# Kernel optimization log

Hardware: AMD Instinct MI355X
Metric: run time of the kernel (lower is better)

## Reference

```python
import jax, jax.numpy as jnp
import numpy as np

STEP = 2  # neighbor window size (init arg `step`)


def _shift_sums(x, step):
    # sum over shifted-left (before) and shifted-right (after) neighbor states,
    # zero-padded at the boundaries, for shifts 1..step. x: [B, L, H]
    before = sum(jnp.pad(x[:, :-s, :], ((0, 0), (s, 0), (0, 0))) for s in range(1, step + 1))
    after = sum(jnp.pad(x[:, s:, :], ((0, 0), (0, s), (0, 0))) for s in range(1, step + 1))
    return before, after


def _slstm_forward(word_inputs, mask, num_layers, init_h, init_c, Wx, Wh, Wi, Wd, b, gWx, gWh, gb):
    B, L, D = word_inputs.shape
    H = Wx.shape[-1]
    fm = mask.astype(word_inputs.dtype)          # [B, L]
    seq_mask = fm[:, :, None]                    # [B, L, 1]
    mask_score = (fm * 1e25 - 1e25)[:, :, None]  # -inf-like for padded positions

    emb = word_inputs * seq_mask                 # embedding_hidden_state_pre
    h = (init_h * 0.1 - 0.05) * seq_mask         # uniform(-0.05, 0.05) init
    c = (init_c * 0.1 - 0.05) * seq_mask
    dh = jnp.mean(h, axis=1)                     # dummy-node hidden [B, H]
    dc = jnp.mean(c, axis=1)                     # dummy-node cell   [B, H]

    for _ in range(num_layers):
        comb = jnp.mean(h, axis=1)               # combined word hidden [B, H]
        dh_rep = jnp.broadcast_to(dh[:, None, :], (B, L, H))
        dc_rep = jnp.broadcast_to(dc[:, None, :], (B, L, H))

        # --- dummy (sentence) node update ---
        g_d = jax.nn.sigmoid(dh @ gWx[0] + comb @ gWh[0] + gb[0])              # [B, H]
        g_o = jax.nn.sigmoid(dh @ gWx[1] + comb @ gWh[1] + gb[1])              # [B, H]
        g_f = jax.nn.sigmoid(dh_rep @ gWx[2] + h @ gWh[2] + gb[2])             # [B, L, H]
        scores = jnp.concatenate([g_f + mask_score, g_d[:, None, :]], axis=1)  # [B, L+1, H]
        scores = jax.nn.softmax(scores, axis=1)
        dummy_c = jnp.sum(scores[:, :L, :] * c, axis=1) + scores[:, L, :] * dc
        dummy_h = g_o * jnp.tanh(dummy_c)

        # --- word node updates ---
        hb, ha = _shift_sums(h, STEP)
        cb, ca = _shift_sums(c, STEP)
        cat_h = jnp.concatenate([hb, ha], axis=-1)  # [B, L, 2H]

        # 7 gates stacked: f1, f2, f3, f4, i, o, u -> pre: [7, B, L, H]
        pre = (jnp.einsum('blh,ghk->gblk', h, Wx)
               + jnp.einsum('blh,ghk->gblk', cat_h, Wh)
               + jnp.einsum('bld,gdk->gblk', emb, Wi)
               + jnp.einsum('blh,ghk->gblk', dh_rep, Wd)
               + b[:, None, None, :])
        sig = jax.nn.sigmoid(pre[:6])
        f1, f2, f3, f4, i_g, o_g = sig[0], sig[1], sig[2], sig[3], sig[4], sig[5]
        u = jnp.tanh(pre[6])

        # normalize the five forget/input gates via softmax across gates
        five = jax.nn.softmax(jnp.stack([f1, f2, f3, f4, i_g], axis=0), axis=0)
        c_new = five[0] * cb + five[1] * ca + five[2] * c + five[3] * dc_rep + five[4] * u
        h_new = o_g * jnp.tanh(c_new)

        h = h_new * seq_mask
        c = c_new * seq_mask
        dh, dc = dummy_h, dummy_c

    return h


def setup_inputs() -> dict:
    key = jax.random.key(0)
    ks = jax.random.split(key, 12)
    B, L, D, H, G = 32, 1024, 256, 256, 7
    s = 0.1  # stddev of param init in the torch module
    return {
        'word_inputs': jax.random.normal(ks[0], (B, L, D), jnp.float32),
        'mask': jnp.ones((B, L), jnp.int32),
        'num_layers': 3,
        'init_h': jax.random.uniform(ks[1], (B, L, H), jnp.float32),
        'init_c': jax.random.uniform(ks[2], (B, L, H), jnp.float32),
        'Wx': jax.random.normal(ks[3], (G, H, H), jnp.float32) * s,
        'Wh': jax.random.normal(ks[4], (G, 2 * H, H), jnp.float32) * s,
        'Wi': jax.random.normal(ks[5], (G, D, H), jnp.float32) * s,
        'Wd': jax.random.normal(ks[6], (G, H, H), jnp.float32) * s,
        'b': jax.random.normal(ks[7], (G, H), jnp.float32) * s,
        'gWx': jax.random.normal(ks[8], (3, H, H), jnp.float32) * s,
        'gWh': jax.random.normal(ks[9], (3, H, H), jnp.float32) * s,
        'gb': jax.random.normal(ks[10], (3, H), jnp.float32) * s,
    }


def reference(word_inputs, mask, num_layers, init_h, init_c, Wx, Wh, Wi, Wd, b, gWx, gWh, gb):
    return _slstm_forward(word_inputs, mask, num_layers, init_h, init_c, Wx, Wh, Wi, Wd, b, gWx, gWh, gb)
```

## Files before the change

kernel.cpp:

```cpp
#include <hip/hip_runtime.h>
#include <hip/hip_bf16.h>
#include <math.h>

#define BB 32
#define LL 1024
#define DD 256
#define HH 256
#define NG 7
#define HW (HH*HH)
#define WhS (2*HH*HH)

typedef short bf16x8 __attribute__((ext_vector_type(8)));
typedef float f32x4  __attribute__((ext_vector_type(4)));
typedef unsigned short u16;
typedef unsigned int u32;

__device__ __forceinline__ float sigm(float x){ return 1.0f/(1.0f + expf(-x)); }
__device__ __forceinline__ float fsig(float x){ return __fdividef(1.0f, 1.0f + __expf(-x)); }
__device__ __forceinline__ float ftanh(float x){ return 1.0f - __fdividef(2.0f, 1.0f + __expf(2.0f*x)); }
__device__ __forceinline__ u16 f2b(float f){
  u32 u = __float_as_uint(f);
  return (u16)((u + 0x7fffu + ((u>>16)&1u)) >> 16);
}
__device__ __forceinline__ float b2f(u16 b){ return __uint_as_float(((u32)b)<<16); }
__device__ __forceinline__ float4 ld4(const float* p){ return *reinterpret_cast<const float4*>(p); }
__device__ __forceinline__ u32 packf2(float lo, float hi){
  float2 s; s.x = lo; s.y = hi;
  __hip_bfloat162 r = __float22bfloat162_rn(s);
  return *reinterpret_cast<u32*>(&r);
}
__device__ __forceinline__ u32 bfadd2(u32 a, u32 b){
  float lo = __uint_as_float(a << 16)        + __uint_as_float(b << 16);
  float hi = __uint_as_float(a & 0xffff0000u) + __uint_as_float(b & 0xffff0000u);
  return packf2(lo, hi);
}

__device__ __forceinline__ void gload16(const void* g, void* l){
  __builtin_amdgcn_global_load_lds(
    (const __attribute__((address_space(1))) unsigned int*)g,
    (__attribute__((address_space(3))) unsigned int*)l, 16, 0, 0);
}
__device__ __forceinline__ f32x4 mfma16(bf16x8 a, bf16x8 b, f32x4 c){
  return __builtin_amdgcn_mfma_f32_16x16x32_bf16(a, b, c, 0, 0, 0);
}

__global__ __launch_bounds__(256) void k_init(const float* __restrict__ ih, const float* __restrict__ ic,
    const int* __restrict__ mask, u16* __restrict__ h, float* __restrict__ c){
  size_t n = (size_t)BB*LL*HH;
  for (size_t idx = (size_t)blockIdx.x*256 + threadIdx.x; idx < n; idx += (size_t)gridDim.x*256){
    float fm = (float)mask[idx>>8];
    h[idx] = f2b((ih[idx]*0.1f - 0.05f)*fm);
    c[idx] = (ic[idx]*0.1f - 0.05f)*fm;
  }
}

__global__ __launch_bounds__(256) void k_embpack(const float* __restrict__ win,
    const int* __restrict__ mask, u16* __restrict__ embp){
  int idx = blockIdx.x*256 + threadIdx.x;
  int m = idx >> 5, c8 = (idx & 31) << 3;
  float fm = (float)mask[m];
  float4 w0 = ld4(win + (size_t)m*DD + c8);
  float4 w1 = ld4(win + (size_t)m*DD + c8 + 4);
  uint4 pv;
  pv.x = packf2(w0.x*fm, w0.y*fm); pv.y = packf2(w0.z*fm, w0.w*fm);
  pv.z = packf2(w1.x*fm, w1.y*fm); pv.w = packf2(w1.z*fm, w1.w*fm);
  *(uint4*)(embp + (size_t)m*HH + c8) = pv;
}

__global__ __launch_bounds__(256) void k_mean1(const u16* __restrict__ h, const float* __restrict__ c,
    float* __restrict__ pmh, float* __restrict__ pmc){
  int b = blockIdx.x, ch = blockIdx.y, k = threadIdx.x;
  const u16* hp = h + ((size_t)b*LL + ch*64)*HH + k;
  const float* cp = c + ((size_t)b*LL + ch*64)*HH + k;
  float sh = 0.f, sc = 0.f;
  for (int l = 0; l < 64; ++l){ sh += b2f(hp[(size_t)l*HH]); sc += cp[(size_t)l*HH]; }
  pmh[(size_t)(b*16+ch)*HH + k] = sh;
  pmc[(size_t)(b*16+ch)*HH + k] = sc;
}
__global__ __launch_bounds__(256) void k_mean2(const float* __restrict__ pmh, const float* __restrict__ pmc,
    float* __restrict__ comb, float* __restrict__ combc){
  int b = blockIdx.x, k = threadIdx.x;
  float sh = 0.f, sc = 0.f;
  for (int ch = 0; ch < 16; ++ch){
    sh += pmh[(size_t)(b*16+ch)*HH + k];
    sc += pmc[(size_t)(b*16+ch)*HH + k];
  }
  comb[b*HH+k]  = sh*(1.0f/LL);
  combc[b*HH+k] = sc*(1.0f/LL);
}

__global__ __launch_bounds__(256) void k_small(const float* __restrict__ dh, const float* __restrict__ comb,
    const float* __restrict__ gWx, const float* __restrict__ gWh, const float* __restrict__ gb,
    const float* __restrict__ Wd, const float* __restrict__ bias,
    float* __restrict__ g_d, float* __restrict__ g_o, float* __restrict__ gx2f, float* __restrict__ wd){
  __shared__ float dsh[HH], csh[HH];
  int b = blockIdx.x, g = blockIdx.y, k = threadIdx.x;
  dsh[k] = dh[b*HH+k]; csh[k] = comb[b*HH+k];
  __syncthreads();
  if (g < NG){
    float aw = bias[g*HH+k];
    const float* W = Wd + (size_t)g*HW + k;
    for (int j = 0; j < HH; ++j) aw += dsh[j]*W[(size_t)j*HH];
    wd[(size_t)(g*BB + b)*HH + k] = aw;
  } else {
    float ad = gb[0*HH+k], ao = gb[1*HH+k], ax = gb[2*HH+k];
    for (int j = 0; j < HH; ++j){
      float dv = dsh[j], cv = csh[j];
      ad += dv*gWx[j*HH+k]      + cv*gWh[j*HH+k];
      ao += dv*gWx[HW + j*HH+k] + cv*gWh[HW + j*HH+k];
      ax += dv*gWx[2*HW + j*HH+k];
    }
    g_d[b*HH+k] = sigm(ad);
    g_o[b*HH+k] = sigm(ao);
    gx2f[b*HH+k] = ax;
  }
}

__global__ __launch_bounds__(256) void k_wpack(const float* __restrict__ Wx, const float* __restrict__ Wh,
    const float* __restrict__ Wi, u16* __restrict__ Bp){
  int idx = blockIdx.x*256 + threadIdx.x;
  int img = idx / 14336, e = idx % 14336;
  int nt = img >> 5, ks = img & 31;
  int g = e >> 11, r = e & 2047;
  int n = r >> 5, kblk = (r>>3)&3, j = r&7;
  int K = ks*32 + kblk*8 + j;
  int N = nt*64 + n;
  int slice = K >> 8, kr = K & 255;
  float v;
  if (slice == 0)      v = Wx[(size_t)g*HW  + (size_t)kr*HH + N];
  else if (slice == 1) v = Wh[(size_t)g*WhS + (size_t)kr*HH + N];
  else if (slice == 2) v = Wh[(size_t)g*WhS + (size_t)(256+kr)*HH + N];
  else                 v = Wi[(size_t)g*HW  + (size_t)kr*HH + N];
  Bp[idx] = f2b(v);
}

__global__ __launch_bounds__(256) void k_gw2pack(const float* __restrict__ gWh, u16* __restrict__ Gp){
  int idx = blockIdx.x*256 + threadIdx.x;
  int img = idx >> 11, r = idx & 2047;
  int nt = img >> 3, ks = img & 7;
  int n = r >> 5, kblk = (r>>3)&3, j = r&7;
  int K = ks*32 + kblk*8 + j, N = nt*64 + n;
  Gp[idx] = f2b(gWh[2*HW + (size_t)K*HH + N]);
}

__global__ __launch_bounds__(256) void k_dummy2(const float* __restrict__ pnumP, const float* __restrict__ pdenP,
    const float* __restrict__ g_d, const float* __restrict__ g_o, const float* __restrict__ dc,
    float* __restrict__ dh_n, float* __restrict__ dc_n){
  int b = blockIdx.x, k = threadIdx.x;
  float num = 0.f, den = 0.f;
  for (int mt = 0; mt < 16; ++mt){
    num += pnumP[(size_t)(b*16+mt)*HH + k];
    den += pdenP[(size_t)(b*16+mt)*HH + k];
  }
  float ed = expf(g_d[b*HH+k]);
  float v = (num + ed*dc[b*HH+k])/(den + ed);
  dc_n[b*HH+k] = v;
  dh_n[b*HH+k] = g_o[b*HH+k]*tanhf(v);
}

__global__ __launch_bounds__(256, 2) void k_main(const u16* __restrict__ h,
    const float* __restrict__ c, const u16* __restrict__ embp,
    const int* __restrict__ mask,
    const u16* __restrict__ Bp, const u16* __restrict__ Gp,
    const float* __restrict__ wd, const float* __restrict__ dc,
    const float* __restrict__ gx2f,
    u16* __restrict__ hout, float* __restrict__ cout, float* __restrict__ hf32,
    float* __restrict__ pnumP, float* __restrict__ pdenP, int wf32, int wc){
  __shared__ __align__(16) unsigned char lsA[3][4][4096];

  int tid = threadIdx.x, lane = tid & 63, wid = tid >> 6;
  int flat = blockIdx.x;
  int xcd = flat & 7, q = flat >> 3;
  int nt  = xcd >> 1;
  int mt  = (xcd & 1)*256 + q;
  int m0 = mt << 6, b = m0 >> 10;
  int li = lane & 15, kg = lane >> 4;

  int rA = wid*16 + (lane>>2); (void)rA;
  int kbA = (lane&3) ^ ((lane>>3)&3);
  int mA = m0 + wid*16 + (lane>>2), lpA = mA & (LL-1);

  int off0 = li*64 + ((kg ^ ((li>>1)&3))<<4);

  const unsigned char* bbase = (const unsigned char*)Bp
      + (size_t)nt*32*28672 + (size_t)(wid*16+li)*64 + (size_t)kg*16;
  const unsigned char* gbase = (const unsigned char*)Gp
      + (size_t)nt*8*4096  + (size_t)(wid*16+li)*64 + (size_t)kg*16;

  f32x4 acc[NG][4];
  f32x4 acc8[4];
  #pragma unroll
  for (int g=0; g<NG; ++g)
    #pragma unroll
    for (int mf=0; mf<4; ++mf) acc[g][mf] = (f32x4)0.f;
  #pragma unroll
  for (int mf=0; mf<4; ++mf) acc8[mf] = (f32x4)0.f;

  auto stage = [&](int Gs, int dst){
    int base = 4*Gs, s1 = base >> 3;
    if (s1 == 0 || s1 == 3){
      const u16* src = (s1 == 0) ? h : embp;
      #pragma unroll
      for (int j=0;j<4;++j)
        gload16(src + (size_t)mA*HH + ((base+j)&7)*32 + kbA*8, lsA[dst][j] + wid*1024);
    } else {
      int d = (s1 == 1) ? -(int)HH : (int)HH;
      bool e1 = (s1 == 1) ? (lpA >= 1) : (lpA <= LL-2);
      bool e2 = (s1 == 1) ? (lpA >= 2) : (lpA <= LL-3);
      #pragma unroll
      for (int j=0;j<4;++j){
        int co = ((base+j)&7)*32 + kbA*8;
        const u16* hp = h + (size_t)mA*HH + co;
        uint4 u1 = e1 ? *(const uint4*)(hp + d)   : make_uint4(0,0,0,0);
        uint4 u2 = e2 ? *(const uint4*)(hp + 2*d) : make_uint4(0,0,0,0);
        uint4 pv;
        pv.x = bfadd2(u1.x,u2.x); pv.y = bfadd2(u1.y,u2.y);
        pv.z = bfadd2(u1.z,u2.z); pv.w = bfadd2(u1.w,u2.w);
        *(uint4*)(lsA[dst][j] + wid*1024 + lane*16) = pv;
      }
    }
  };

  stage(0, 0);
  stage(1, 1);
  asm volatile("s_waitcnt vmcnt(4)" ::: "memory");
  __builtin_amdgcn_s_barrier();

  #pragma unroll 1
  for (int G = 0; G < 8; ++G){
    if (G < 6) stage(G+2, (G+2)%3);
    int setc = G % 3;
    #pragma unroll
    for (int j = 0; j < 4; ++j){
      int ks = 4*G + j;
      const unsigned char* bstep = bbase + (size_t)ks*28672;
      bf16x8 bg[NG];
      #pragma unroll
      for (int g = 0; g < NG; ++g) bg[g] = *(const bf16x8*)(bstep + g*4096);
      bf16x8 aa[4];
      #pragma unroll
      for (int mf=0; mf<4; ++mf)
        aa[mf] = *(const bf16x8*)(lsA[setc][j] + mf*1024 + off0);
      __builtin_amdgcn_s_setprio(1);
      #pragma unroll
      for (int g = 0; g < NG; ++g)
        #pragma unroll
        for (int mf=0; mf<4; ++mf) acc[g][mf] = mfma16(aa[mf], bg[g], acc[g][mf]);
      if (ks < 8){
        bf16x8 b8 = *(const bf16x8*)(gbase + (size_t)ks*4096);
        #pragma unroll
        for (int mf=0; mf<4; ++mf) acc8[mf] = mfma16(aa[mf], b8, acc8[mf]);
      }
      __builtin_amdgcn_s_setprio(0);
    }
    asm volatile("s_waitcnt vmcnt(4)" ::: "memory");
    __builtin_amdgcn_s_barrier();
  }

  int col = nt*64 + wid*16 + li;
  float wdv[NG];
  #pragma unroll
  for (int g=0; g<NG; ++g) wdv[g] = wd[(size_t)(g*BB+b)*HH + col];
  float dcv = dc[b*HH + col];
  float gx  = gx2f[b*HH + col];
  float num = 0.f, den = 0.f;

  #pragma unroll
  for (int mf=0; mf<4; ++mf)
  #pragma unroll
  for (int j=0; j<4; ++j){
    int m = m0 + mf*16 + kg*4 + j;
    int lp = m & (LL-1);
    float fm = (float)mask[m];
    const float* cp = c + (size_t)m*HH + col;
    float cc = cp[0];
    float cbv = 0.f, cav = 0.f;
    if (lp >= 1)    cbv += cp[-(int)HH];
    if (lp >= 2)    cbv += cp[-2*(int)HH];
    if (lp <= LL-2) cav += cp[HH];
    if (lp <= LL-3) cav += cp[2*HH];
    float s0 = fsig(acc[0][mf][j] + wdv[0]);
    float s1 = fsig(acc[1][mf][j] + wdv[1]);
    float s2 = fsig(acc[2][mf][j] + wdv[2]);
    float s3 = fsig(acc[3][mf][j] + wdv[3]);
    float s4 = fsig(acc[4][mf][j] + wdv[4]);
    float s5 = fsig(acc[5][mf][j] + wdv[5]);
    float u  = ftanh(acc[6][mf][j] + wdv[6]);
    float e0 = __expf(s0), e1 = __expf(s1), e2 = __expf(s2), e3 = __expf(s3), e4 = __expf(s4);
    float inv = __fdividef(1.0f, e0+e1+e2+e3+e4);
    float cn = (e0*cbv + e1*cav + e2*cc + e3*dcv + e4*u)*inv;
    float hn = s5*ftanh(cn);
    hout[(size_t)m*HH + col] = f2b(hn*fm);
    if (wc)   cout[(size_t)m*HH + col] = cn*fm;
    if (wf32) hf32[(size_t)m*HH + col] = hn*fm;
    float s8 = fsig(acc8[mf][j] + gx);
    float e8 = fm * __expf(s8);
    num += e8 * cc;
    den += e8;
  }
  num += __shfl_xor(num, 16); num += __shfl_xor(num, 32);
  den += __shfl_xor(den, 16); den += __shfl_xor(den, 32);
  if (kg == 0){
    pnumP[(size_t)(m0>>6)*HH + col] = num;
    pdenP[(size_t)(m0>>6)*HH + col] = den;
  }
}

extern "C" void kernel_launch(void* const* d_in, const int* in_sizes, int n_in,
                              void* d_out, int out_size, void* d_ws, size_t ws_size,
                              hipStream_t stream) {
  const float* win   = (const float*)d_in[0];
  const int*   mask  = (const int*)d_in[1];
  const float* ih    = (const float*)d_in[3];
  const float* ic    = (const float*)d_in[4];
  const float* Wx    = (const float*)d_in[5];
  const float* Wh    = (const float*)d_in[6];
  const float* Wi    = (const float*)d_in[7];
  const float* Wd    = (const float*)d_in[8];
  const float* bias  = (const float*)d_in[9];
  const float* gWx   = (const float*)d_in[10];
  const float* gWh   = (const float*)d_in[11];
  const float* gb    = (const float*)d_in[12];

  const size_t SZ = (size_t)BB*LL*HH;
  char* p = (char*)d_ws;
  auto alloc = [&](size_t bytes)->char*{ char* r = p; p += (bytes + 255) & ~(size_t)255; return r; };
  u16*   hA    = (u16*)  alloc(SZ*2);
  u16*   hB    = (u16*)  alloc(SZ*2);
  float* cA    = (float*)alloc(SZ*4);
  float* cB    = (float*)d_out;
  u16*   embp  = (u16*)  alloc(SZ*2);
  u16*   Bp    = (u16*)  alloc((size_t)1835008*2);
  u16*   Gp    = (u16*)  alloc((size_t)65536*2);
  float* comb  = (float*)alloc(BB*HH*4);
  float* combc = (float*)alloc(BB*HH*4);
  float* dh0   = (float*)alloc(BB*HH*4);
  float* dh1   = (float*)alloc(BB*HH*4);
  float* dc0   = (float*)alloc(BB*HH*4);
  float* dc1   = (float*)alloc(BB*HH*4);
  float* g_d   = (float*)alloc(BB*HH*4);
  float* g_o   = (float*)alloc(BB*HH*4);
  float* gx2f  = (float*)alloc(BB*HH*4);
  float* wd    = (float*)alloc((size_t)NG*BB*HH*4);
  float* pnumP = (float*)alloc((size_t)512*HH*4);
  float* pdenP = (float*)alloc((size_t)512*HH*4);
  float* pmh   = (float*)alloc((size_t)BB*16*HH*4);
  float* pmc   = (float*)alloc((size_t)BB*16*HH*4);
  float* dhb[2] = {dh0, dh1};
  float* dcb[2] = {dc0, dc1};

  k_wpack<<<7168, 256, 0, stream>>>(Wx, Wh, Wi, Bp);
  k_gw2pack<<<256, 256, 0, stream>>>(gWh, Gp);
  k_embpack<<<4096, 256, 0, stream>>>(win, mask, embp);
  k_init<<<2048, 256, 0, stream>>>(ih, ic, mask, hA, cA);

  u16 *h_cur = hA, *h_nxt = hB;
  float *c_cur = cA, *c_nxt = cB;
  for (int layer = 0; layer < 3; ++layer){
    k_mean1<<<dim3(BB,16), 256, 0, stream>>>(h_cur, c_cur, pmh, pmc);
    k_mean2<<<BB, 256, 0, stream>>>(pmh, pmc, comb, combc);
    const float* dh_l = (layer == 0) ? comb  : dhb[(layer+1)&1];
    const float* dc_l = (layer == 0) ? combc : dcb[(layer+1)&1];
    k_small<<<dim3(BB,8), 256, 0, stream>>>(dh_l, comb, gWx, gWh, gb, Wd, bias, g_d, g_o, gx2f, wd);
    int last = (layer == 2);
    k_main<<<2048, 256, 0, stream>>>(h_cur, c_cur, embp, mask, Bp, Gp, wd, dc_l, gx2f,
                                     h_nxt, c_nxt, (float*)d_out, pnumP, pdenP, last, !last);
    k_dummy2<<<BB, 256, 0, stream>>>(pnumP, pdenP, g_d, g_o, dc_l, dhb[layer&1], dcb[layer&1]);
    u16* th = h_cur; h_cur = h_nxt; h_nxt = th;
    float* tc = c_cur; c_cur = c_nxt; c_nxt = tc;
  }
}
```

Baseline: 694.9 us.

## Fuse sequence-mean reductions into init and main kernels, drop mean kernels

Column partial sums of h and c over sequence positions are now produced inside k_init and in the k_main epilogue through wave shuffles, so the separate k_mean1/k_mean2 passes that reread the full h and c tensors each layer are gone. The final reduction of the partials moves into the small gate kernel, now k_ms. This saves a full read of h (bf16) and c (fp32) per layer plus two launches. In exchange k_main gets two extra shuffle reductions and stores, and the layer-1+ mean is summed from fp32 values rather than from rounded bf16 h, which changes numerics slightly.

```diff
diff --git a/kernel.cpp b/kernel.cpp
--- a/kernel.cpp
+++ b/kernel.cpp
@@ -45,13 +45,22 @@
 }
 
 __global__ __launch_bounds__(256) void k_init(const float* __restrict__ ih, const float* __restrict__ ic,
-    const int* __restrict__ mask, u16* __restrict__ h, float* __restrict__ c){
-  size_t n = (size_t)BB*LL*HH;
-  for (size_t idx = (size_t)blockIdx.x*256 + threadIdx.x; idx < n; idx += (size_t)gridDim.x*256){
-    float fm = (float)mask[idx>>8];
-    h[idx] = f2b((ih[idx]*0.1f - 0.05f)*fm);
-    c[idx] = (ic[idx]*0.1f - 0.05f)*fm;
-  }
+    const int* __restrict__ mask, u16* __restrict__ h, float* __restrict__ c,
+    float* __restrict__ pmh, float* __restrict__ pmc){
+  int b = blockIdx.x, ch = blockIdx.y, k = threadIdx.x;
+  size_t base = ((size_t)b*LL + ch*64)*HH + k;
+  float sh = 0.f, sc = 0.f;
+  for (int l = 0; l < 64; ++l){
+    size_t idx = base + (size_t)l*HH;
+    float fm = (float)mask[b*LL + ch*64 + l];
+    float hv = (ih[idx]*0.1f - 0.05f)*fm;
+    float cv = (ic[idx]*0.1f - 0.05f)*fm;
+    h[idx] = f2b(hv);
+    c[idx] = cv;
+    sh += hv; sc += cv;
+  }
+  pmh[(size_t)(b*16+ch)*HH + k] = sh;
+  pmc[(size_t)(b*16+ch)*HH + k] = sc;
 }
 
 __global__ __launch_bounds__(256) void k_embpack(const float* __restrict__ win,
@@ -67,35 +76,19 @@
   *(uint4*)(embp + (size_t)m*HH + c8) = pv;
 }
 
-__global__ __launch_bounds__(256) void k_mean1(const u16* __restrict__ h, const float* __restrict__ c,
-    float* __restrict__ pmh, float* __restrict__ pmc){
-  int b = blockIdx.x, ch = blockIdx.y, k = threadIdx.x;
-  const u16* hp = h + ((size_t)b*LL + ch*64)*HH + k;
-  const float* cp = c + ((size_t)b*LL + ch*64)*HH + k;
-  float sh = 0.f, sc = 0.f;
-  for (int l = 0; l < 64; ++l){ sh += b2f(hp[(size_t)l*HH]); sc += cp[(size_t)l*HH]; }
-  pmh[(size_t)(b*16+ch)*HH + k] = sh;
-  pmc[(size_t)(b*16+ch)*HH + k] = sc;
-}
-__global__ __launch_bounds__(256) void k_mean2(const float* __restrict__ pmh, const float* __restrict__ pmc,
-    float* __restrict__ comb, float* __restrict__ combc){
-  int b = blockIdx.x, k = threadIdx.x;
-  float sh = 0.f, sc = 0.f;
-  for (int ch = 0; ch < 16; ++ch){
-    sh += pmh[(size_t)(b*16+ch)*HH + k];
-    sc += pmc[(size_t)(b*16+ch)*HH + k];
-  }
-  comb[b*HH+k]  = sh*(1.0f/LL);
-  combc[b*HH+k] = sc*(1.0f/LL);
-}
-
-__global__ __launch_bounds__(256) void k_small(const float* __restrict__ dh, const float* __restrict__ comb,
+__global__ __launch_bounds__(256) void k_ms(const float* __restrict__ pmh, const float* __restrict__ pmc,
+    const float* __restrict__ dh_in,
     const float* __restrict__ gWx, const float* __restrict__ gWh, const float* __restrict__ gb,
     const float* __restrict__ Wd, const float* __restrict__ bias,
-    float* __restrict__ g_d, float* __restrict__ g_o, float* __restrict__ gx2f, float* __restrict__ wd){
+    float* __restrict__ g_d, float* __restrict__ g_o, float* __restrict__ gx2f, float* __restrict__ wd,
+    float* __restrict__ combc_out, int l0flag){
   __shared__ float dsh[HH], csh[HH];
   int b = blockIdx.x, g = blockIdx.y, k = threadIdx.x;
-  dsh[k] = dh[b*HH+k]; csh[k] = comb[b*HH+k];
+  float sh = 0.f;
+  for (int ch = 0; ch < 16; ++ch) sh += pmh[(size_t)(b*16+ch)*HH + k];
+  float comb = sh*(1.0f/LL);
+  csh[k] = comb;
+  dsh[k] = l0flag ? comb : dh_in[b*HH+k];
   __syncthreads();
   if (g < NG){
     float aw = bias[g*HH+k];
@@ -113,6 +106,11 @@
     g_d[b*HH+k] = sigm(ad);
     g_o[b*HH+k] = sigm(ao);
     gx2f[b*HH+k] = ax;
+    if (l0flag){
+      float sc = 0.f;
+      for (int ch = 0; ch < 16; ++ch) sc += pmc[(size_t)(b*16+ch)*HH + k];
+      combc_out[b*HH+k] = sc*(1.0f/LL);
+    }
   }
 }
 
@@ -165,7 +163,8 @@
     const float* __restrict__ wd, const float* __restrict__ dc,
     const float* __restrict__ gx2f,
     u16* __restrict__ hout, float* __restrict__ cout, float* __restrict__ hf32,
-    float* __restrict__ pnumP, float* __restrict__ pdenP, int wf32, int wc){
+    float* __restrict__ pnumP, float* __restrict__ pdenP,
+    float* __restrict__ pmh, float* __restrict__ pmc, int wf32, int wc){
   __shared__ __align__(16) unsigned char lsA[3][4][4096];
 
   int tid = threadIdx.x, lane = tid & 63, wid = tid >> 6;
@@ -176,7 +175,6 @@
   int m0 = mt << 6, b = m0 >> 10;
   int li = lane & 15, kg = lane >> 4;
 
-  int rA = wid*16 + (lane>>2); (void)rA;
   int kbA = (lane&3) ^ ((lane>>3)&3);
   int mA = m0 + wid*16 + (lane>>2), lpA = mA & (LL-1);
 
@@ -263,7 +261,7 @@
   for (int g=0; g<NG; ++g) wdv[g] = wd[(size_t)(g*BB+b)*HH + col];
   float dcv = dc[b*HH + col];
   float gx  = gx2f[b*HH + col];
-  float num = 0.f, den = 0.f;
+  float num = 0.f, den = 0.f, msh = 0.f, msc = 0.f;
 
   #pragma unroll
   for (int mf=0; mf<4; ++mf)
@@ -290,19 +288,26 @@
     float inv = __fdividef(1.0f, e0+e1+e2+e3+e4);
     float cn = (e0*cbv + e1*cav + e2*cc + e3*dcv + e4*u)*inv;
     float hn = s5*ftanh(cn);
-    hout[(size_t)m*HH + col] = f2b(hn*fm);
-    if (wc)   cout[(size_t)m*HH + col] = cn*fm;
-    if (wf32) hf32[(size_t)m*HH + col] = hn*fm;
+    float ho = hn*fm, co = cn*fm;
+    hout[(size_t)m*HH + col] = f2b(ho);
+    if (wc)   cout[(size_t)m*HH + col] = co;
+    if (wf32) hf32[(size_t)m*HH + col] = ho;
     float s8 = fsig(acc8[mf][j] + gx);
     float e8 = fm * __expf(s8);
     num += e8 * cc;
     den += e8;
+    msh += ho; msc += co;
   }
   num += __shfl_xor(num, 16); num += __shfl_xor(num, 32);
   den += __shfl_xor(den, 16); den += __shfl_xor(den, 32);
+  msh += __shfl_xor(msh, 16); msh += __shfl_xor(msh, 32);
+  msc += __shfl_xor(msc, 16); msc += __shfl_xor(msc, 32);
   if (kg == 0){
-    pnumP[(size_t)(m0>>6)*HH + col] = num;
-    pdenP[(size_t)(m0>>6)*HH + col] = den;
+    size_t tix = (size_t)(m0>>6)*HH + col;
+    pnumP[tix] = num;
+    pdenP[tix] = den;
+    pmh[tix]   = msh;
+    pmc[tix]   = msc;
   }
 }
 
@@ -332,7 +337,6 @@
   u16*   embp  = (u16*)  alloc(SZ*2);
   u16*   Bp    = (u16*)  alloc((size_t)1835008*2);
   u16*   Gp    = (u16*)  alloc((size_t)65536*2);
-  float* comb  = (float*)alloc(BB*HH*4);
   float* combc = (float*)alloc(BB*HH*4);
   float* dh0   = (float*)alloc(BB*HH*4);
   float* dh1   = (float*)alloc(BB*HH*4);
@@ -344,27 +348,28 @@
   float* wd    = (float*)alloc((size_t)NG*BB*HH*4);
   float* pnumP = (float*)alloc((size_t)512*HH*4);
   float* pdenP = (float*)alloc((size_t)512*HH*4);
-  float* pmh   = (float*)alloc((size_t)BB*16*HH*4);
-  float* pmc   = (float*)alloc((size_t)BB*16*HH*4);
+  float* pmh   = (float*)alloc((size_t)512*HH*4);
+  float* pmc   = (float*)alloc((size_t)512*HH*4);
   float* dhb[2] = {dh0, dh1};
   float* dcb[2] = {dc0, dc1};
 
   k_wpack<<<7168, 256, 0, stream>>>(Wx, Wh, Wi, Bp);
   k_gw2pack<<<256, 256, 0, stream>>>(gWh, Gp);
   k_embpack<<<4096, 256, 0, stream>>>(win, mask, embp);
-  k_init<<<2048, 256, 0, stream>>>(ih, ic, mask, hA, cA);
+  k_init<<<dim3(BB,16), 256, 0, stream>>>(ih, ic, mask, hA, cA, pmh, pmc);
 
   u16 *h_cur = hA, *h_nxt = hB;
   float *c_cur = cA, *c_nxt = cB;
   for (int layer = 0; layer < 3; ++layer){
-    k_mean1<<<dim3(BB,16), 256, 0, stream>>>(h_cur, c_cur, pmh, pmc);
-    k_mean2<<<BB, 256, 0, stream>>>(pmh, pmc, comb, combc);
-    const float* dh_l = (layer == 0) ? comb  : dhb[(layer+1)&1];
-    const float* dc_l = (layer == 0) ? combc : dcb[(layer+1)&1];
-    k_small<<<dim3(BB,8), 256, 0, stream>>>(dh_l, comb, gWx, gWh, gb, Wd, bias, g_d, g_o, gx2f, wd);
+    int l0 = (layer == 0);
+    const float* dh_l = l0 ? (const float*)nullptr : dhb[(layer+1)&1];
+    const float* dc_l = l0 ? combc : dcb[(layer+1)&1];
+    k_ms<<<dim3(BB,8), 256, 0, stream>>>(pmh, pmc, dh_l, gWx, gWh, gb, Wd, bias,
+                                         g_d, g_o, gx2f, wd, combc, l0);
     int last = (layer == 2);
     k_main<<<2048, 256, 0, stream>>>(h_cur, c_cur, embp, mask, Bp, Gp, wd, dc_l, gx2f,
-                                     h_nxt, c_nxt, (float*)d_out, pnumP, pdenP, last, !last);
+                                     h_nxt, c_nxt, (float*)d_out, pnumP, pdenP,
+                                     pmh, pmc, last, !last);
     k_dummy2<<<BB, 256, 0, stream>>>(pnumP, pdenP, g_d, g_o, dc_l, dhb[layer&1], dcb[layer&1]);
     u16* th = h_cur; h_cur = h_nxt; h_nxt = th;
     float* tc = c_cur; c_cur = c_nxt; c_nxt = tc;
```

Result: faster. 665.9 us (median of 2 runs) (-4.2%).
